# Optimization experiments

Hardware: AMD Instinct MI355X
Metric: run time of the kernel (lower is better)

Reference implementation:

```python
import jax, jax.numpy as jnp
import numpy as np

N_TREE = 200
DEPTH = 3
N_LEAF = 2 ** (DEPTH + 1) - 1      # 15 internal decision nodes
N_LEAVES = N_LEAF + 1              # 16 leaves
N_NODE = 64
BATCH = 2048
D_FEAT = 512
LR = 0.01


def _leaf_paths(depth):
    """For each of the 2^(depth+1) leaves, the internal-node index and the
    left/right bit at every level (matches the tf.gather index construction:
    bit==0 -> take p, bit==1 -> take 1-p; children of node n are 2n+1, 2n+2)."""
    L = 2 ** (depth + 1)
    nodes = np.zeros((L, depth + 1), np.int32)
    bits = np.zeros((L, depth + 1), np.int32)
    for l in range(L):
        node = 0
        for d in range(depth + 1):
            bit = (l >> (depth - d)) & 1
            nodes[l, d] = node
            bits[l, d] = bit
            node = 2 * node + 1 + bit
    return nodes, bits

_NODES, _BITS = _leaf_paths(DEPTH)


def setup_inputs() -> dict:
    key = jax.random.key(0)
    ks = jax.random.split(key, 9)
    u = lambda k, s: jax.random.uniform(k, s, jnp.float32, -0.05, 0.05)  # keras 'uniform' init
    return {
        "x": jax.random.normal(ks[0], (BATCH, D_FEAT), jnp.float32),
        "y_true": jax.random.normal(ks[1], (BATCH, 1), jnp.float32),
        "w_t": u(ks[2], (N_TREE, D_FEAT, N_NODE)),
        "b_t": u(ks[3], (N_TREE, N_NODE)),
        "w_d": u(ks[4], (N_TREE, N_NODE, N_LEAF)),
        "b_d": u(ks[5], (N_TREE, N_LEAF)),
        "w_l": u(ks[6], (N_TREE, N_LEAVES)),
        "b_l": u(ks[7], (N_TREE,)),
        "f_0": jnp.full((1,), 0.5, jnp.float32),
    }


def reference(x, y_true, w_t, b_t, w_d, b_d, w_l, b_l, f_0):
    B = x.shape[0]
    # Batched per-tree small MLP (the 200-iteration Python loop in the original).
    # Dropout is identity at inference.
    h = jax.nn.relu(jnp.einsum('bd,tdn->tbn', x, w_t) + b_t[:, None, :])        # [T,B,N_NODE]
    p = jax.nn.sigmoid(jnp.einsum('tbn,tnl->tbl', h, w_d) + b_d[:, None, :])    # [T,B,15]
    # Soft binary-tree routing: mu[t,b,leaf] = prod over path of p or (1-p).
    # This reproduces the tiled-index tf.gather construction exactly.
    pn = p[..., _NODES]                                                         # [T,B,16,DEPTH+1]
    q = jnp.where(_BITS == 1, 1.0 - pn, pn)
    mu = jnp.prod(q, axis=-1)                                                   # [T,B,16]
    # Per-tree leaf score with tanh.
    f = jnp.tanh(jnp.einsum('tbl,tl->tb', mu, w_l) + b_l[:, None])              # [T,B]
    # Sequential boosting accumulation: predict_k = f_0 + lr * sum_{i<k} f_i.
    cum = f_0 + LR * jnp.cumsum(f.T, axis=1)                                    # [B,T]
    py_x = jnp.concatenate([jnp.broadcast_to(f_0[None, :], (B, 1)), cum], axis=1)  # [B,T+1]
    return py_x
```

## Files before the change

### kernel.cpp

```cpp
#include <hip/hip_runtime.h>

#define T_TREES 200
#define BATCH   2048
#define D_FEAT  512
#define N_NODE  64
#define LR      0.01f

typedef __attribute__((__ext_vector_type__(8)))  __bf16 bf16x8;
typedef __attribute__((__ext_vector_type__(16))) float  f32x16;

__device__ __forceinline__ unsigned short f32_to_bf16(float f) {
    unsigned u = __float_as_uint(f);
    u += 0x7FFFu + ((u >> 16) & 1u);
    return (unsigned short)(u >> 16);
}

__device__ __forceinline__ void gload_lds16(const void* g, void* l) {
    __builtin_amdgcn_global_load_lds(
        (__attribute__((address_space(1))) void*)(void*)g,
        (__attribute__((address_space(3))) void*)l,
        16, 0, 0);
}

__global__ __launch_bounds__(256) void prep_all(
    const float* __restrict__ x, const float* __restrict__ w_t,
    const float* __restrict__ w_d,
    unsigned short* __restrict__ x_p, unsigned short* __restrict__ w_p,
    unsigned short* __restrict__ w_dt) {
    __shared__ float tile[64 * 65];
    int b = blockIdx.x;
    if (b < 256) {
        int mb = b >> 3, slab = b & 7;
        const float* src = x + (mb * 64) * D_FEAT + slab * 64;
        #pragma unroll
        for (int p = 0; p < 16; ++p) {
            int idx = p * 256 + threadIdx.x;
            int r = idx >> 6, c = idx & 63;
            tile[r * 65 + c] = src[r * D_FEAT + c];
        }
        __syncthreads();
        int mt = mb >> 1, mq = mb & 1;
        unsigned short* dst = x_p + mt * 65536 + slab * 8192 + mq * 512;
        #pragma unroll
        for (int p = 0; p < 8; ++p) {
            int idx = p * 256 + threadIdx.x;
            int kgl = idx >> 8;
            int r   = (idx >> 2) & 63;
            int jp  = idx & 3;
            ushort2 o;
            o.x = f32_to_bf16(tile[r * 65 + kgl * 8 + jp * 2]);
            o.y = f32_to_bf16(tile[r * 65 + kgl * 8 + jp * 2 + 1]);
            *(ushort2*)(dst + kgl * 1024 + r * 8 + jp * 2) = o;
        }
    } else if (b < 1856) {
        int bb = b - 256;
        int t = bb >> 3, slab = bb & 7;
        const float* src = w_t + t * (D_FEAT * N_NODE) + slab * 64 * N_NODE;
        #pragma unroll
        for (int p = 0; p < 16; ++p) {
            int idx = p * 256 + threadIdx.x;
            int d = idx >> 6, n = idx & 63;
            tile[d * 65 + n] = src[d * N_NODE + n];
        }
        __syncthreads();
        unsigned short* dst = w_p + (t >> 1) * 65536 + slab * 8192 + (t & 1) * 512;
        #pragma unroll
        for (int p = 0; p < 8; ++p) {
            int idx = p * 256 + threadIdx.x;
            int kgl = idx >> 8;
            int n   = (idx >> 2) & 63;
            int jp  = idx & 3;
            ushort2 o;
            o.x = f32_to_bf16(tile[(kgl * 8 + jp * 2) * 65 + n]);
            o.y = f32_to_bf16(tile[(kgl * 8 + jp * 2 + 1) * 65 + n]);
            *(ushort2*)(dst + kgl * 1024 + n * 8 + jp * 2) = o;
        }
    } else {
        int i = (b - 1856) * 256 + threadIdx.x;
        int n = i & 63;
        int l = (i >> 6) & 31;
        int t = i >> 11;
        float v = (l < 15) ? w_d[(t * 64 + n) * 15 + l] : 0.f;
        w_dt[i] = f32_to_bf16(v);
    }
}

__global__ __launch_bounds__(256, 4) void gbdt_main(
    const unsigned short* __restrict__ x_p,
    const unsigned short* __restrict__ w_p,
    const unsigned short* __restrict__ w_dt,
    const float* __restrict__ b_t,
    const float* __restrict__ b_d,
    const float* __restrict__ w_l,
    const float* __restrict__ b_l,
    float* __restrict__ f_ws)
{
    __shared__ alignas(16) char smem[34816];
    unsigned short* Hs = (unsigned short*)smem;
    float*          Pf = (float*)smem;

    const int tid    = threadIdx.x;
    const int lane   = tid & 63;
    const int w      = tid >> 6;
    const int lane31 = lane & 31;
    const int kh     = lane >> 5;
    const int wm     = w >> 1;
    const int wn     = w & 1;

    const int xcd  = blockIdx.x & 7;
    const int slot = blockIdx.x >> 3;
    const int mt   = slot & 15;
    const int pj   = slot >> 4;
    const int pair = xcd * 13 + pj;
    if (pair >= 100) return;
    const int t0 = pair * 2;
    const int m0 = mt * 128;

    const unsigned short* pA = x_p + mt * 65536 + kh * 1024 + (wm * 64 + lane31) * 8;
    const char* gb = (const char*)(w_p + pair * 65536) + tid * 16;

    f32x16 acc[2][2];
    #pragma unroll
    for (int mb = 0; mb < 2; ++mb)
        #pragma unroll
        for (int nb = 0; nb < 2; ++nb)
            acc[mb][nb] = (f32x16)(0.f);

    bf16x8 a_cur[4], a_nxt[4];
    #pragma unroll
    for (int s2 = 0; s2 < 2; ++s2)
        #pragma unroll
        for (int mb = 0; mb < 2; ++mb)
            a_cur[s2 * 2 + mb] = *(const bf16x8*)(pA + s2 * 2048 + mb * 256);
    gload_lds16(gb, smem + tid * 16);
    gload_lds16(gb + 4096, smem + tid * 16 + 4096);

    for (int c = 0; c < 16; ++c) {
        __syncthreads();
        if (c < 15) {
            char* nx = smem + ((c + 1) & 1) * 8192;
            gload_lds16(gb + (c + 1) * 8192, nx + tid * 16);
            gload_lds16(gb + (c + 1) * 8192 + 4096, nx + tid * 16 + 4096);
            #pragma unroll
            for (int s2 = 0; s2 < 2; ++s2)
                #pragma unroll
                for (int mb = 0; mb < 2; ++mb)
                    a_nxt[s2 * 2 + mb] =
                        *(const bf16x8*)(pA + (c + 1) * 4096 + s2 * 2048 + mb * 256);
        }
        const char* buf = smem + (c & 1) * 8192;
        #pragma unroll
        for (int s2 = 0; s2 < 2; ++s2) {
            const int kgl = 2 * s2 + kh;
            bf16x8 bv[2];
            #pragma unroll
            for (int nb = 0; nb < 2; ++nb)
                bv[nb] = *(const bf16x8*)(buf + (kgl * 128 + wn * 64 + nb * 32 + lane31) * 16);
            #pragma unroll
            for (int mb = 0; mb < 2; ++mb)
                #pragma unroll
                for (int nb = 0; nb < 2; ++nb)
                    acc[mb][nb] = __builtin_amdgcn_mfma_f32_32x32x16_bf16(
                        a_cur[s2 * 2 + mb], bv[nb], acc[mb][nb], 0, 0, 0);
        }
        #pragma unroll
        for (int i = 0; i < 4; ++i) a_cur[i] = a_nxt[i];
    }

    __syncthreads();

    #pragma unroll
    for (int nb = 0; nb < 2; ++nb) {
        float btv = b_t[(t0 + wn) * 64 + nb * 32 + lane31];
        #pragma unroll
        for (int mb = 0; mb < 2; ++mb)
            #pragma unroll
            for (int r = 0; r < 16; ++r) {
                int m = wm * 64 + mb * 32 + (r & 3) + 8 * (r >> 2) + 4 * kh;
                float h = fmaxf(acc[mb][nb][r] + btv, 0.f);
                Hs[wn * 8704 + m * 68 + nb * 32 + lane31] = f32_to_bf16(h);
            }
    }
    __syncthreads();

    f32x16 acc2[2] = { (f32x16)(0.f), (f32x16)(0.f) };
    const unsigned short* pW = w_dt + (t0 + wn) * 2048 + lane31 * 64 + kh * 8;
    #pragma unroll
    for (int s = 0; s < 4; ++s) {
        bf16x8 bv = *(const bf16x8*)(pW + s * 16);
        #pragma unroll
        for (int i = 0; i < 2; ++i) {
            const unsigned short* pH =
                Hs + wn * 8704 + (wm * 64 + i * 32 + lane31) * 68 + s * 16 + kh * 8;
            bf16x8 av = *(const bf16x8*)pH;
            acc2[i] = __builtin_amdgcn_mfma_f32_32x32x16_bf16(av, bv, acc2[i], 0, 0, 0);
        }
    }
    __syncthreads();

    if (lane31 < 15) {
        float bdv = b_d[(t0 + wn) * 15 + lane31];
        #pragma unroll
        for (int i = 0; i < 2; ++i)
            #pragma unroll
            for (int r = 0; r < 16; ++r) {
                int m = wm * 64 + i * 32 + (r & 3) + 8 * (r >> 2) + 4 * kh;
                float lg = acc2[i][r] + bdv;
                Pf[(wn * 128 + m) * 17 + lane31] = 1.f / (1.f + __expf(-lg));
            }
    }
    __syncthreads();

    {
        int m = tid & 127;
        int j = tid >> 7;
        int t = t0 + j;
        float pv[15];
        #pragma unroll
        for (int i = 0; i < 15; ++i) pv[i] = Pf[(j * 128 + m) * 17 + i];
        float facc = 0.f;
        #pragma unroll
        for (int leaf = 0; leaf < 16; ++leaf) {
            float mu = 1.f;
            int node = 0;
            #pragma unroll
            for (int d = 0; d < 4; ++d) {
                int bit = (leaf >> (3 - d)) & 1;
                float p = pv[node];
                mu *= bit ? (1.f - p) : p;
                node = 2 * node + 1 + bit;
            }
            facc += mu * w_l[t * 16 + leaf];
        }
        f_ws[(m0 + m) * T_TREES + t] = tanhf(facc + b_l[t]);
    }
}

__global__ void scan_k(const float* __restrict__ f_ws, const float* __restrict__ f0p,
                       float* __restrict__ out) {
    int b = blockIdx.x, tid = threadIdx.x;
    int lane = tid & 63, wid = tid >> 6;
    float f0 = f0p[0];
    float x = (tid < T_TREES) ? f_ws[b * T_TREES + tid] : 0.f;
    #pragma unroll
    for (int off = 1; off < 64; off <<= 1) {
        float y = __shfl_up(x, off, 64);
        if (lane >= off) x += y;
    }
    __shared__ float wsum[4];
    if (lane == 63) wsum[wid] = x;
    __syncthreads();
    float base = 0.f;
    for (int i = 0; i < wid; ++i) base += wsum[i];
    float incl = x + base;
    if (tid == 0) out[b * (T_TREES + 1)] = f0;
    if (tid < T_TREES) out[b * (T_TREES + 1) + 1 + tid] = f0 + LR * incl;
}

extern "C" void kernel_launch(void* const* d_in, const int* in_sizes, int n_in,
                              void* d_out, int out_size, void* d_ws, size_t ws_size,
                              hipStream_t stream) {
    const float* x   = (const float*)d_in[0];
    const float* w_t = (const float*)d_in[2];
    const float* b_t = (const float*)d_in[3];
    const float* w_d = (const float*)d_in[4];
    const float* b_d = (const float*)d_in[5];
    const float* w_l = (const float*)d_in[6];
    const float* b_l = (const float*)d_in[7];
    const float* f_0 = (const float*)d_in[8];
    float* out = (float*)d_out;

    char* ws = (char*)d_ws;
    unsigned short* x_p  = (unsigned short*)(ws);
    unsigned short* w_p  = (unsigned short*)(ws + 2097152);
    unsigned short* w_dt = (unsigned short*)(ws + 15204352);
    float*          f_ws = (float*)(ws + 16023552);

    prep_all<<<3456, 256, 0, stream>>>(x, w_t, w_d, x_p, w_p, w_dt);
    gbdt_main<<<1664, 256, 0, stream>>>(x_p, w_p, w_dt, b_t, b_d, w_l, b_l, f_ws);
    scan_k<<<BATCH, 256, 0, stream>>>(f_ws, f_0, out);
}
```

Measured before the change: 131.3 us.

## Vectorize prep stores, unroll GEMM pipeline with setprio, wave-per-row scan

The prep kernel now writes each packed bf16 group as one 16-byte store using hardware bf16 conversion, in place of several 4-byte stores. The main GEMM loop is manually unrolled by two with explicit ping-pong buffers, dropping the register copy of the next A fragment, and MFMA sections are wrapped in s_setprio. The scan kernel handles one batch row per wavefront with float4 loads and a single wave shuffle scan, removing shared memory and block barriers and launching a quarter as many blocks. The hardware bf16 cast may round differently from the manual rounding in some cases.

```diff
diff --git a/kernel.cpp b/kernel.cpp
--- a/kernel.cpp
+++ b/kernel.cpp
@@ -42,15 +42,15 @@
         int mt = mb >> 1, mq = mb & 1;
         unsigned short* dst = x_p + mt * 65536 + slab * 8192 + mq * 512;
         #pragma unroll
-        for (int p = 0; p < 8; ++p) {
-            int idx = p * 256 + threadIdx.x;
-            int kgl = idx >> 8;
-            int r   = (idx >> 2) & 63;
-            int jp  = idx & 3;
-            ushort2 o;
-            o.x = f32_to_bf16(tile[r * 65 + kgl * 8 + jp * 2]);
-            o.y = f32_to_bf16(tile[r * 65 + kgl * 8 + jp * 2 + 1]);
-            *(ushort2*)(dst + kgl * 1024 + r * 8 + jp * 2) = o;
+        for (int p = 0; p < 2; ++p) {
+            int sid = p * 256 + threadIdx.x;
+            int kgl = sid >> 6;
+            int r   = sid & 63;
+            const float* sr = &tile[r * 65 + kgl * 8];
+            bf16x8 o;
+            #pragma unroll
+            for (int j = 0; j < 8; ++j) o[j] = (__bf16)sr[j];
+            *(bf16x8*)(dst + kgl * 1024 + r * 8) = o;
         }
     } else if (b < 1856) {
         int bb = b - 256;
@@ -65,15 +65,14 @@
         __syncthreads();
         unsigned short* dst = w_p + (t >> 1) * 65536 + slab * 8192 + (t & 1) * 512;
         #pragma unroll
-        for (int p = 0; p < 8; ++p) {
-            int idx = p * 256 + threadIdx.x;
-            int kgl = idx >> 8;
-            int n   = (idx >> 2) & 63;
-            int jp  = idx & 3;
-            ushort2 o;
-            o.x = f32_to_bf16(tile[(kgl * 8 + jp * 2) * 65 + n]);
-            o.y = f32_to_bf16(tile[(kgl * 8 + jp * 2 + 1) * 65 + n]);
-            *(ushort2*)(dst + kgl * 1024 + n * 8 + jp * 2) = o;
+        for (int p = 0; p < 2; ++p) {
+            int sid = p * 256 + threadIdx.x;
+            int kgl = sid >> 6;
+            int n   = sid & 63;
+            bf16x8 o;
+            #pragma unroll
+            for (int j = 0; j < 8; ++j) o[j] = (__bf16)tile[(kgl * 8 + j) * 65 + n];
+            *(bf16x8*)(dst + kgl * 1024 + n * 8) = o;
         }
     } else {
         int i = (b - 1856) * 256 + threadIdx.x;
@@ -97,6 +96,7 @@
 {
     __shared__ alignas(16) char smem[34816];
     unsigned short* Hs = (unsigned short*)smem;
+    __bf16*         Hb = (__bf16*)smem;
     float*          Pf = (float*)smem;
 
     const int tid    = threadIdx.x;
@@ -126,46 +126,58 @@
         for (int nb = 0; nb < 2; ++nb)
             acc[mb][nb] = (f32x16)(0.f);
 
-    bf16x8 a_cur[4], a_nxt[4];
-    #pragma unroll
-    for (int s2 = 0; s2 < 2; ++s2)
-        #pragma unroll
-        for (int mb = 0; mb < 2; ++mb)
-            a_cur[s2 * 2 + mb] = *(const bf16x8*)(pA + s2 * 2048 + mb * 256);
-    gload_lds16(gb, smem + tid * 16);
-    gload_lds16(gb + 4096, smem + tid * 16 + 4096);
-
-    for (int c = 0; c < 16; ++c) {
+#define STAGE_B(cn, bufdst) do {                                   \
+        gload_lds16(gb + (cn) * 8192, (bufdst) + tid * 16);        \
+        gload_lds16(gb + (cn) * 8192 + 4096, (bufdst) + tid * 16 + 4096); \
+    } while (0)
+
+#define LOAD_A(cn, areg) do {                                      \
+        _Pragma("unroll")                                          \
+        for (int s2 = 0; s2 < 2; ++s2)                             \
+            _Pragma("unroll")                                      \
+            for (int mb = 0; mb < 2; ++mb)                         \
+                (areg)[s2 * 2 + mb] =                              \
+                    *(const bf16x8*)(pA + (cn) * 4096 + s2 * 2048 + mb * 256); \
+    } while (0)
+
+#define COMPUTE(bufsrc, areg) do {                                 \
+        __builtin_amdgcn_s_setprio(1);                             \
+        _Pragma("unroll")                                          \
+        for (int s2 = 0; s2 < 2; ++s2) {                           \
+            const int kgl = 2 * s2 + kh;                           \
+            bf16x8 bv0 = *(const bf16x8*)((bufsrc) + (kgl * 128 + wn * 64 + 0 * 32 + lane31) * 16); \
+            bf16x8 bv1 = *(const bf16x8*)((bufsrc) + (kgl * 128 + wn * 64 + 1 * 32 + lane31) * 16); \
+            acc[0][0] = __builtin_amdgcn_mfma_f32_32x32x16_bf16((areg)[s2 * 2 + 0], bv0, acc[0][0], 0, 0, 0); \
+            acc[0][1] = __builtin_amdgcn_mfma_f32_32x32x16_bf16((areg)[s2 * 2 + 0], bv1, acc[0][1], 0, 0, 0); \
+            acc[1][0] = __builtin_amdgcn_mfma_f32_32x32x16_bf16((areg)[s2 * 2 + 1], bv0, acc[1][0], 0, 0, 0); \
+            acc[1][1] = __builtin_amdgcn_mfma_f32_32x32x16_bf16((areg)[s2 * 2 + 1], bv1, acc[1][1], 0, 0, 0); \
+        }                                                          \
+        __builtin_amdgcn_s_setprio(0);                             \
+    } while (0)
+
+    char* buf0 = smem;
+    char* buf1 = smem + 8192;
+
+    bf16x8 aA[4], aB[4];
+    LOAD_A(0, aA);
+    STAGE_B(0, buf0);
+
+    for (int cc = 0; cc < 14; cc += 2) {
         __syncthreads();
-        if (c < 15) {
-            char* nx = smem + ((c + 1) & 1) * 8192;
-            gload_lds16(gb + (c + 1) * 8192, nx + tid * 16);
-            gload_lds16(gb + (c + 1) * 8192 + 4096, nx + tid * 16 + 4096);
-            #pragma unroll
-            for (int s2 = 0; s2 < 2; ++s2)
-                #pragma unroll
-                for (int mb = 0; mb < 2; ++mb)
-                    a_nxt[s2 * 2 + mb] =
-                        *(const bf16x8*)(pA + (c + 1) * 4096 + s2 * 2048 + mb * 256);
-        }
-        const char* buf = smem + (c & 1) * 8192;
-        #pragma unroll
-        for (int s2 = 0; s2 < 2; ++s2) {
-            const int kgl = 2 * s2 + kh;
-            bf16x8 bv[2];
-            #pragma unroll
-            for (int nb = 0; nb < 2; ++nb)
-                bv[nb] = *(const bf16x8*)(buf + (kgl * 128 + wn * 64 + nb * 32 + lane31) * 16);
-            #pragma unroll
-            for (int mb = 0; mb < 2; ++mb)
-                #pragma unroll
-                for (int nb = 0; nb < 2; ++nb)
-                    acc[mb][nb] = __builtin_amdgcn_mfma_f32_32x32x16_bf16(
-                        a_cur[s2 * 2 + mb], bv[nb], acc[mb][nb], 0, 0, 0);
-        }
-        #pragma unroll
-        for (int i = 0; i < 4; ++i) a_cur[i] = a_nxt[i];
-    }
+        STAGE_B(cc + 1, buf1);
+        LOAD_A(cc + 1, aB);
+        COMPUTE(buf0, aA);
+        __syncthreads();
+        STAGE_B(cc + 2, buf0);
+        LOAD_A(cc + 2, aA);
+        COMPUTE(buf1, aB);
+    }
+    __syncthreads();
+    STAGE_B(15, buf1);
+    LOAD_A(15, aB);
+    COMPUTE(buf0, aA);
+    __syncthreads();
+    COMPUTE(buf1, aB);
 
     __syncthreads();
 
@@ -178,13 +190,14 @@
             for (int r = 0; r < 16; ++r) {
                 int m = wm * 64 + mb * 32 + (r & 3) + 8 * (r >> 2) + 4 * kh;
                 float h = fmaxf(acc[mb][nb][r] + btv, 0.f);
-                Hs[wn * 8704 + m * 68 + nb * 32 + lane31] = f32_to_bf16(h);
+                Hb[wn * 8704 + m * 68 + nb * 32 + lane31] = (__bf16)h;
             }
     }
     __syncthreads();
 
     f32x16 acc2[2] = { (f32x16)(0.f), (f32x16)(0.f) };
     const unsigned short* pW = w_dt + (t0 + wn) * 2048 + lane31 * 64 + kh * 8;
+    __builtin_amdgcn_s_setprio(1);
     #pragma unroll
     for (int s = 0; s < 4; ++s) {
         bf16x8 bv = *(const bf16x8*)(pW + s * 16);
@@ -196,6 +209,7 @@
             acc2[i] = __builtin_amdgcn_mfma_f32_32x32x16_bf16(av, bv, acc2[i], 0, 0, 0);
         }
     }
+    __builtin_amdgcn_s_setprio(0);
     __syncthreads();
 
     if (lane31 < 15) {
@@ -234,27 +248,39 @@
         }
         f_ws[(m0 + m) * T_TREES + t] = tanhf(facc + b_l[t]);
     }
-}
-
-__global__ void scan_k(const float* __restrict__ f_ws, const float* __restrict__ f0p,
-                       float* __restrict__ out) {
-    int b = blockIdx.x, tid = threadIdx.x;
-    int lane = tid & 63, wid = tid >> 6;
+#undef STAGE_B
+#undef LOAD_A
+#undef COMPUTE
+}
+
+__global__ __launch_bounds__(256) void scan_k(const float* __restrict__ f_ws,
+                                              const float* __restrict__ f0p,
+                                              float* __restrict__ out) {
+    int lane = threadIdx.x & 63, wid = threadIdx.x >> 6;
+    int b = blockIdx.x * 4 + wid;
     float f0 = f0p[0];
-    float x = (tid < T_TREES) ? f_ws[b * T_TREES + tid] : 0.f;
+    float4 v;
+    if (lane < 50) v = *(const float4*)(f_ws + b * T_TREES + lane * 4);
+    else           v = make_float4(0.f, 0.f, 0.f, 0.f);
+    float p0 = v.x;
+    float p1 = p0 + v.y;
+    float p2 = p1 + v.z;
+    float p3 = p2 + v.w;
+    float s = p3;
     #pragma unroll
     for (int off = 1; off < 64; off <<= 1) {
-        float y = __shfl_up(x, off, 64);
-        if (lane >= off) x += y;
-    }
-    __shared__ float wsum[4];
-    if (lane == 63) wsum[wid] = x;
-    __syncthreads();
-    float base = 0.f;
-    for (int i = 0; i < wid; ++i) base += wsum[i];
-    float incl = x + base;
-    if (tid == 0) out[b * (T_TREES + 1)] = f0;
-    if (tid < T_TREES) out[b * (T_TREES + 1) + 1 + tid] = f0 + LR * incl;
+        float y = __shfl_up(s, off, 64);
+        if (lane >= off) s += y;
+    }
+    float excl = s - p3;
+    if (lane < 50) {
+        float* o = out + b * (T_TREES + 1) + 1 + lane * 4;
+        o[0] = f0 + LR * (excl + p0);
+        o[1] = f0 + LR * (excl + p1);
+        o[2] = f0 + LR * (excl + p2);
+        o[3] = f0 + LR * (excl + p3);
+    }
+    if (lane == 0) out[b * (T_TREES + 1)] = f0;
 }
 
 extern "C" void kernel_launch(void* const* d_in, const int* in_sizes, int n_in,
@@ -278,5 +304,5 @@
 
     prep_all<<<3456, 256, 0, stream>>>(x, w_t, w_d, x_p, w_p, w_dt);
     gbdt_main<<<1664, 256, 0, stream>>>(x_p, w_p, w_dt, b_t, b_d, w_l, b_l, f_ws);
-    scan_k<<<BATCH, 256, 0, stream>>>(f_ws, f_0, out);
-}
+    scan_k<<<512, 256, 0, stream>>>(f_ws, f_0, out);
+}
```

New measurement: 130.0 us. No clear change (-1.1%).
